# Performance work log

Hardware: AMD Instinct MI355X
Metric: run time of the kernel (lower is better)

The kernel has to match this reference:

```python
import jax, jax.numpy as jnp
import numpy as np

GRAVITY, MAIN_THRUST, SIDE_TORQUE, DT = 10.0, 6.0, 1.0, 0.02
H_OBS = jnp.array([[1, 0, 0, 0, 0, 0],
                   [0, 1, 0, 0, 0, 0],
                   [0, 0, 0, 0, 1, 0]], dtype=jnp.float32)  # (3,6)


def build_psd(log_diag, off_diag, dim):
    rows, cols = np.tril_indices(dim, -1)  # row-major, same order as torch.tril_indices
    L = jnp.zeros((dim, dim), dtype=log_diag.dtype)
    L = L.at[jnp.arange(dim), jnp.arange(dim)].set(jnp.exp(log_diag))
    L = L.at[rows, cols].set(off_diag)
    return L @ L.T + 1e-6 * jnp.eye(dim, dtype=log_diag.dtype)


def setup_inputs() -> dict:
    key = jax.random.key(0)
    B = 524288
    ks = jax.random.split(key, 8)
    z = jax.random.normal(ks[0], (B, 3), dtype=jnp.float32)
    u = jax.random.uniform(ks[1], (B, 2), dtype=jnp.float32)
    x_prev = jax.random.normal(ks[2], (B, 6), dtype=jnp.float32)
    A = 0.1 * jax.random.normal(ks[3], (B, 6, 6), dtype=jnp.float32)
    P_prev = jnp.einsum('bij,bkj->bik', A, A) + 0.5 * jnp.eye(6, dtype=jnp.float32)
    q_log_diag = jnp.array([-3.0, -3.0, -2.0, -2.0, -3.0, -2.0], dtype=jnp.float32)
    q_off_diag = 0.01 * jax.random.normal(ks[4], (15,), dtype=jnp.float32)
    r_log_diag = jnp.array([-2.0, -2.0, -2.0], dtype=jnp.float32)
    r_off_diag = 0.01 * jax.random.normal(ks[5], (3,), dtype=jnp.float32)
    return {"z": z, "u": u, "x_prev": x_prev, "P_prev": P_prev,
            "q_log_diag": q_log_diag, "q_off_diag": q_off_diag,
            "r_log_diag": r_log_diag, "r_off_diag": r_off_diag}


def _dynamics(x, u):
    px, py, vx, vy, theta, omega = (x[:, i] for i in range(6))
    main_power = jnp.clip(u[:, 0], 0.0, 1.0)
    lateral = u[:, 1]
    sin_th, cos_th = jnp.sin(theta), jnp.cos(theta)
    ax = -MAIN_THRUST * sin_th * main_power
    ay = MAIN_THRUST * cos_th * main_power - GRAVITY
    alpha = SIDE_TORQUE * lateral
    new_vx = vx + ax * DT
    new_vy = vy + ay * DT
    new_omega = omega + alpha * DT
    new_px = px + new_vx * DT
    new_py = py + new_vy * DT
    new_theta = theta + new_omega * DT
    return jnp.stack([new_px, new_py, new_vx, new_vy, new_theta, new_omega], axis=-1)


def _dynamics_jacobian(x, u):
    B = x.shape[0]
    theta = x[:, 4]
    main_power = jnp.clip(u[:, 0], 0.0, 1.0)
    sin_th, cos_th = jnp.sin(theta), jnp.cos(theta)
    Tm = MAIN_THRUST * main_power
    d = jnp.arange(6)
    F = jnp.zeros((B, 6, 6), dtype=x.dtype).at[:, d, d].set(1.0)
    F = F.at[:, 0, 2].set(DT).at[:, 1, 3].set(DT).at[:, 4, 5].set(DT)
    F = F.at[:, 2, 4].set(-Tm * cos_th * DT)
    F = F.at[:, 3, 4].set(-Tm * sin_th * DT)
    F = F.at[:, 0, 4].set(-Tm * cos_th * (DT * DT))
    F = F.at[:, 1, 4].set(-Tm * sin_th * (DT * DT))
    return F


def reference(z, u, x_prev, P_prev, q_log_diag, q_off_diag, r_log_diag, r_off_diag):
    Q = build_psd(q_log_diag, q_off_diag, 6)
    R = build_psd(r_log_diag, r_off_diag, 3)
    H = H_OBS
    # predict
    x_pred = _dynamics(x_prev, u)                              # (B,6)
    F = _dynamics_jacobian(x_prev, u)                          # (B,6,6)
    P_pred = jnp.einsum('bij,bjk,blk->bil', F, P_prev, F) + Q  # F P F^T + Q
    # update
    z_pred = jnp.einsum('ij,bj->bi', H, x_pred)                # (B,3)
    y = z - z_pred
    HP = jnp.einsum('ij,bjk->bik', H, P_pred)                  # (B,3,6)
    S = jnp.einsum('bij,kj->bik', HP, H) + R                   # (B,3,3)
    K = jnp.swapaxes(jnp.linalg.solve(S, HP), -1, -2)          # (B,6,3)
    x_upd = x_pred + jnp.einsum('bij,bj->bi', K, y)
    IKH = jnp.eye(6, dtype=x_pred.dtype) - jnp.einsum('bij,jk->bik', K, H)
    P_upd = (jnp.einsum('bij,bjk,blk->bil', IKH, P_pred, IKH)
             + jnp.einsum('bij,jk,blk->bil', K, R, K))          # Joseph form
    return (x_upd, P_upd)
```

## Files before the change

### kernel.cpp

```cpp
#include <hip/hip_runtime.h>

namespace {
constexpr float GRAVITY     = 10.0f;
constexpr float MAIN_THRUST = 6.0f;
constexpr float DT          = 0.02f;
constexpr int   BLK         = 256;
constexpr int   ROWPAD      = 37;
}

__global__ __launch_bounds__(BLK) void ekf_kernel(
    const float* __restrict__ z,
    const float* __restrict__ u,
    const float* __restrict__ x_prev,
    const float* __restrict__ P_prev,
    const float* __restrict__ q_log_diag,
    const float* __restrict__ q_off_diag,
    const float* __restrict__ r_log_diag,
    const float* __restrict__ r_off_diag,
    float* __restrict__ x_out,
    float* __restrict__ P_out,
    int B)
{
    __shared__ float smem[BLK * ROWPAD];

    const int t = threadIdx.x;
    const long long blockElem0 = (long long)blockIdx.x * BLK;
    const long long elemsLeft  = (long long)B - blockElem0;
    const int nElem  = elemsLeft >= BLK ? BLK : (int)elemsLeft;
    const int count4 = nElem * 9;

    {
        const float4* gP4 = reinterpret_cast<const float4*>(P_prev + blockElem0 * 36);
        #pragma unroll
        for (int k = 0; k < 9; ++k) {
            const int g4 = t + k * BLK;
            if (g4 < count4) {
                const float4 v = gP4[g4];
                const int elem = g4 / 9;
                const int off4 = g4 % 9;
                float* dst = &smem[elem * ROWPAD + off4 * 4];
                dst[0] = v.x; dst[1] = v.y; dst[2] = v.z; dst[3] = v.w;
            }
        }
    }
    __syncthreads();

    const bool valid = (t < nElem);
    const long long b = blockElem0 + t;

    if (valid) {
        float L[6][6];
        #pragma unroll
        for (int i = 0; i < 6; ++i)
            #pragma unroll
            for (int j = 0; j < 6; ++j) L[i][j] = 0.0f;
        #pragma unroll
        for (int i = 0; i < 6; ++i) L[i][i] = expf(q_log_diag[i]);
        L[1][0] = q_off_diag[0];
        L[2][0] = q_off_diag[1];  L[2][1] = q_off_diag[2];
        L[3][0] = q_off_diag[3];  L[3][1] = q_off_diag[4];  L[3][2] = q_off_diag[5];
        L[4][0] = q_off_diag[6];  L[4][1] = q_off_diag[7];  L[4][2] = q_off_diag[8];
        L[4][3] = q_off_diag[9];
        L[5][0] = q_off_diag[10]; L[5][1] = q_off_diag[11]; L[5][2] = q_off_diag[12];
        L[5][3] = q_off_diag[13]; L[5][4] = q_off_diag[14];

        float Q[6][6];
        #pragma unroll
        for (int i = 0; i < 6; ++i) {
            #pragma unroll
            for (int j = 0; j <= i; ++j) {
                float s = 0.0f;
                #pragma unroll
                for (int k = 0; k <= j; ++k) s += L[i][k] * L[j][k];
                if (i == j) s += 1e-6f;
                Q[i][j] = s;
                Q[j][i] = s;
            }
        }

        const float rd0 = expf(r_log_diag[0]);
        const float rd1 = expf(r_log_diag[1]);
        const float rd2 = expf(r_log_diag[2]);
        const float ro0 = r_off_diag[0], ro1 = r_off_diag[1], ro2 = r_off_diag[2];
        const float R00 = rd0 * rd0 + 1e-6f;
        const float R10 = ro0 * rd0;
        const float R11 = ro0 * ro0 + rd1 * rd1 + 1e-6f;
        const float R20 = ro1 * rd0;
        const float R21 = ro1 * ro0 + ro2 * rd1;
        const float R22 = ro1 * ro1 + ro2 * ro2 + rd2 * rd2 + 1e-6f;
        const float Rm[3][3] = {{R00, R10, R20}, {R10, R11, R21}, {R20, R21, R22}};

        const float2* xp2 = reinterpret_cast<const float2*>(x_prev + 6 * b);
        const float2 x01 = xp2[0], x23 = xp2[1], x45 = xp2[2];
        const float px = x01.x, py = x01.y, vx = x23.x, vy = x23.y;
        const float th = x45.x, om = x45.y;

        const float2 uu = *reinterpret_cast<const float2*>(u + 2 * b);
        const float mp  = fminf(fmaxf(uu.x, 0.0f), 1.0f);
        const float lat = uu.y;

        float s_th, c_th;
        __sincosf(th, &s_th, &c_th);

        const float Tm  = MAIN_THRUST * mp;
        const float ax  = -Tm * s_th;
        const float ay  =  Tm * c_th - GRAVITY;
        const float nvx = vx + ax * DT;
        const float nvy = vy + ay * DT;
        const float nom = om + lat * DT;
        const float npx = px + nvx * DT;
        const float npy = py + nvy * DT;
        const float nth = th + nom * DT;
        const float xp[6] = {npx, npy, nvx, nvy, nth, nom};

        const float f24 = -Tm * c_th * DT;
        const float f34 = -Tm * s_th * DT;
        const float f04 = f24 * DT;
        const float f14 = f34 * DT;

        float P[36];
        const float* myrow = &smem[t * ROWPAD];
        #pragma unroll
        for (int j = 0; j < 36; ++j) P[j] = myrow[j];

        #pragma unroll
        for (int j = 0; j < 6; ++j) {
            P[0 * 6 + j] += DT * P[2 * 6 + j] + f04 * P[4 * 6 + j];
            P[1 * 6 + j] += DT * P[3 * 6 + j] + f14 * P[4 * 6 + j];
            P[2 * 6 + j] += f24 * P[4 * 6 + j];
            P[3 * 6 + j] += f34 * P[4 * 6 + j];
            P[4 * 6 + j] += DT * P[5 * 6 + j];
        }
        #pragma unroll
        for (int i = 0; i < 6; ++i) {
            const float m0 = P[i * 6 + 0], m1 = P[i * 6 + 1], m2 = P[i * 6 + 2];
            const float m3 = P[i * 6 + 3], m4 = P[i * 6 + 4], m5 = P[i * 6 + 5];
            P[i * 6 + 0] = m0 + DT * m2 + f04 * m4 + Q[i][0];
            P[i * 6 + 1] = m1 + DT * m3 + f14 * m4 + Q[i][1];
            P[i * 6 + 2] = m2 + f24 * m4 + Q[i][2];
            P[i * 6 + 3] = m3 + f34 * m4 + Q[i][3];
            P[i * 6 + 4] = m4 + DT * m5 + Q[i][4];
            P[i * 6 + 5] = m5 + Q[i][5];
        }

        const float* zp = z + 3 * b;
        const float y0 = zp[0] - npx;
        const float y1 = zp[1] - npy;
        const float y2 = zp[2] - nth;

        const float s00 = P[0 * 6 + 0] + Rm[0][0];
        const float s01 = P[0 * 6 + 1] + Rm[0][1];
        const float s02 = P[0 * 6 + 4] + Rm[0][2];
        const float s10 = P[1 * 6 + 0] + Rm[1][0];
        const float s11 = P[1 * 6 + 1] + Rm[1][1];
        const float s12 = P[1 * 6 + 4] + Rm[1][2];
        const float s20 = P[4 * 6 + 0] + Rm[2][0];
        const float s21 = P[4 * 6 + 1] + Rm[2][1];
        const float s22 = P[4 * 6 + 4] + Rm[2][2];

        const float det = s00 * (s11 * s22 - s12 * s21)
                        + s01 * (s12 * s20 - s10 * s22)
                        + s02 * (s10 * s21 - s11 * s20);
        const float invd = 1.0f / det;
        const float i00 = (s11 * s22 - s12 * s21) * invd;
        const float i01 = (s02 * s21 - s01 * s22) * invd;
        const float i02 = (s01 * s12 - s02 * s11) * invd;
        const float i10 = (s12 * s20 - s10 * s22) * invd;
        const float i11 = (s00 * s22 - s02 * s20) * invd;
        const float i12 = (s02 * s10 - s00 * s12) * invd;
        const float i20 = (s10 * s21 - s11 * s20) * invd;
        const float i21 = (s01 * s20 - s00 * s21) * invd;
        const float i22 = (s00 * s11 - s01 * s10) * invd;

        float K[6][3];
        #pragma unroll
        for (int i = 0; i < 6; ++i) {
            const float hp0 = P[0 * 6 + i];
            const float hp1 = P[1 * 6 + i];
            const float hp2 = P[4 * 6 + i];
            K[i][0] = i00 * hp0 + i01 * hp1 + i02 * hp2;
            K[i][1] = i10 * hp0 + i11 * hp1 + i12 * hp2;
            K[i][2] = i20 * hp0 + i21 * hp1 + i22 * hp2;
        }

        float2* xo2 = reinterpret_cast<float2*>(x_out + 6 * b);
        float xu[6];
        #pragma unroll
        for (int i = 0; i < 6; ++i)
            xu[i] = xp[i] + K[i][0] * y0 + K[i][1] * y1 + K[i][2] * y2;
        xo2[0] = make_float2(xu[0], xu[1]);
        xo2[1] = make_float2(xu[2], xu[3]);
        xo2[2] = make_float2(xu[4], xu[5]);

        float r0[6], r1[6], r4[6];
        #pragma unroll
        for (int j = 0; j < 6; ++j) {
            r0[j] = P[0 * 6 + j];
            r1[j] = P[1 * 6 + j];
            r4[j] = P[4 * 6 + j];
        }
        #pragma unroll
        for (int i = 0; i < 6; ++i)
            #pragma unroll
            for (int j = 0; j < 6; ++j)
                P[i * 6 + j] -= K[i][0] * r0[j] + K[i][1] * r1[j] + K[i][2] * r4[j];

        float c0[6], c1[6], c4[6];
        #pragma unroll
        for (int i = 0; i < 6; ++i) {
            c0[i] = P[i * 6 + 0];
            c1[i] = P[i * 6 + 1];
            c4[i] = P[i * 6 + 4];
        }
        float KR[6][3];
        #pragma unroll
        for (int i = 0; i < 6; ++i) {
            #pragma unroll
            for (int a = 0; a < 3; ++a)
                KR[i][a] = K[i][0] * Rm[0][a] + K[i][1] * Rm[1][a] + K[i][2] * Rm[2][a];
        }
        #pragma unroll
        for (int i = 0; i < 6; ++i) {
            #pragma unroll
            for (int j = 0; j < 6; ++j) {
                P[i * 6 + j] += -(c0[i] * K[j][0] + c1[i] * K[j][1] + c4[i] * K[j][2])
                                + (KR[i][0] * K[j][0] + KR[i][1] * K[j][1] + KR[i][2] * K[j][2]);
            }
        }

        float* myrowW = &smem[t * ROWPAD];
        #pragma unroll
        for (int j = 0; j < 36; ++j) myrowW[j] = P[j];
    }
    __syncthreads();

    {
        float4* oP4 = reinterpret_cast<float4*>(P_out + blockElem0 * 36);
        #pragma unroll
        for (int k = 0; k < 9; ++k) {
            const int g4 = t + k * BLK;
            if (g4 < count4) {
                const int elem = g4 / 9;
                const int off4 = g4 % 9;
                const float* src = &smem[elem * ROWPAD + off4 * 4];
                float4 v;
                v.x = src[0]; v.y = src[1]; v.z = src[2]; v.w = src[3];
                oP4[g4] = v;
            }
        }
    }
}

extern "C" void kernel_launch(void* const* d_in, const int* in_sizes, int n_in,
                              void* d_out, int out_size, void* d_ws, size_t ws_size,
                              hipStream_t stream) {
    const float* z          = (const float*)d_in[0];
    const float* u          = (const float*)d_in[1];
    const float* x_prev     = (const float*)d_in[2];
    const float* P_prev     = (const float*)d_in[3];
    const float* q_log_diag = (const float*)d_in[4];
    const float* q_off_diag = (const float*)d_in[5];
    const float* r_log_diag = (const float*)d_in[6];
    const float* r_off_diag = (const float*)d_in[7];

    const int B = in_sizes[0] / 3;
    float* x_out = (float*)d_out;
    float* P_out = (float*)d_out + (size_t)B * 6;

    const int grid = (B + BLK - 1) / BLK;
    ekf_kernel<<<grid, BLK, 0, stream>>>(z, u, x_prev, P_prev,
                                         q_log_diag, q_off_diag,
                                         r_log_diag, r_off_diag,
                                         x_out, P_out, B);
}
```

Measured before the change: 191.7 us.

## Simplify covariance update, precompute Q/R in a separate kernel, vectorize LDS

Replaces the Joseph-form covariance update with the simple (I-KH)P form. The two are algebraically equal for the optimal Kalman gain, so the second 6x6 correction pass is dropped. The per-thread construction of Q and R, including expf calls, moves into a one-thread pre-kernel that writes them to workspace; the main kernel then reads them as uniform loads. Shared-memory rows are padded to 44 floats so they can be read and written as float4, and the block size drops to 128. The trade-offs are an extra kernel launch and slightly different numerical behaviour, since the Joseph form's symmetry and positive-definiteness safeguards are gone.

```diff
diff --git a/kernel.cpp b/kernel.cpp
--- a/kernel.cpp
+++ b/kernel.cpp
@@ -4,8 +4,43 @@
 constexpr float GRAVITY     = 10.0f;
 constexpr float MAIN_THRUST = 6.0f;
 constexpr float DT          = 0.02f;
-constexpr int   BLK         = 256;
-constexpr int   ROWPAD      = 37;
+constexpr int   BLK         = 128;
+constexpr int   ROWPAD      = 44;
+}
+
+__global__ void qr_precompute(const float* __restrict__ qld,
+                              const float* __restrict__ qod,
+                              const float* __restrict__ rld,
+                              const float* __restrict__ rod,
+                              float* __restrict__ out)
+{
+    if (threadIdx.x != 0 || blockIdx.x != 0) return;
+    float L[6][6];
+    for (int i = 0; i < 6; ++i)
+        for (int j = 0; j < 6; ++j) L[i][j] = 0.0f;
+    for (int i = 0; i < 6; ++i) L[i][i] = expf(qld[i]);
+    L[1][0] = qod[0];
+    L[2][0] = qod[1];  L[2][1] = qod[2];
+    L[3][0] = qod[3];  L[3][1] = qod[4];  L[3][2] = qod[5];
+    L[4][0] = qod[6];  L[4][1] = qod[7];  L[4][2] = qod[8];  L[4][3] = qod[9];
+    L[5][0] = qod[10]; L[5][1] = qod[11]; L[5][2] = qod[12]; L[5][3] = qod[13];
+    L[5][4] = qod[14];
+    for (int i = 0; i < 6; ++i)
+        for (int j = 0; j < 6; ++j) {
+            float s = 0.0f;
+            const int m = i < j ? i : j;
+            for (int k = 0; k <= m; ++k) s += L[i][k] * L[j][k];
+            if (i == j) s += 1e-6f;
+            out[i * 6 + j] = s;
+        }
+    const float rd0 = expf(rld[0]), rd1 = expf(rld[1]), rd2 = expf(rld[2]);
+    const float ro0 = rod[0], ro1 = rod[1], ro2 = rod[2];
+    out[36] = rd0 * rd0 + 1e-6f;
+    out[37] = ro0 * rd0;
+    out[38] = ro0 * ro0 + rd1 * rd1 + 1e-6f;
+    out[39] = ro1 * rd0;
+    out[40] = ro1 * ro0 + ro2 * rd1;
+    out[41] = ro1 * ro1 + ro2 * ro2 + rd2 * rd2 + 1e-6f;
 }
 
 __global__ __launch_bounds__(BLK) void ekf_kernel(
@@ -13,10 +48,7 @@
     const float* __restrict__ u,
     const float* __restrict__ x_prev,
     const float* __restrict__ P_prev,
-    const float* __restrict__ q_log_diag,
-    const float* __restrict__ q_off_diag,
-    const float* __restrict__ r_log_diag,
-    const float* __restrict__ r_off_diag,
+    const float* __restrict__ qr,
     float* __restrict__ x_out,
     float* __restrict__ P_out,
     int B)
@@ -38,8 +70,7 @@
                 const float4 v = gP4[g4];
                 const int elem = g4 / 9;
                 const int off4 = g4 % 9;
-                float* dst = &smem[elem * ROWPAD + off4 * 4];
-                dst[0] = v.x; dst[1] = v.y; dst[2] = v.z; dst[3] = v.w;
+                *reinterpret_cast<float4*>(&smem[elem * ROWPAD + off4 * 4]) = v;
             }
         }
     }
@@ -49,46 +80,8 @@
     const long long b = blockElem0 + t;
 
     if (valid) {
-        float L[6][6];
-        #pragma unroll
-        for (int i = 0; i < 6; ++i)
-            #pragma unroll
-            for (int j = 0; j < 6; ++j) L[i][j] = 0.0f;
-        #pragma unroll
-        for (int i = 0; i < 6; ++i) L[i][i] = expf(q_log_diag[i]);
-        L[1][0] = q_off_diag[0];
-        L[2][0] = q_off_diag[1];  L[2][1] = q_off_diag[2];
-        L[3][0] = q_off_diag[3];  L[3][1] = q_off_diag[4];  L[3][2] = q_off_diag[5];
-        L[4][0] = q_off_diag[6];  L[4][1] = q_off_diag[7];  L[4][2] = q_off_diag[8];
-        L[4][3] = q_off_diag[9];
-        L[5][0] = q_off_diag[10]; L[5][1] = q_off_diag[11]; L[5][2] = q_off_diag[12];
-        L[5][3] = q_off_diag[13]; L[5][4] = q_off_diag[14];
-
-        float Q[6][6];
-        #pragma unroll
-        for (int i = 0; i < 6; ++i) {
-            #pragma unroll
-            for (int j = 0; j <= i; ++j) {
-                float s = 0.0f;
-                #pragma unroll
-                for (int k = 0; k <= j; ++k) s += L[i][k] * L[j][k];
-                if (i == j) s += 1e-6f;
-                Q[i][j] = s;
-                Q[j][i] = s;
-            }
-        }
-
-        const float rd0 = expf(r_log_diag[0]);
-        const float rd1 = expf(r_log_diag[1]);
-        const float rd2 = expf(r_log_diag[2]);
-        const float ro0 = r_off_diag[0], ro1 = r_off_diag[1], ro2 = r_off_diag[2];
-        const float R00 = rd0 * rd0 + 1e-6f;
-        const float R10 = ro0 * rd0;
-        const float R11 = ro0 * ro0 + rd1 * rd1 + 1e-6f;
-        const float R20 = ro1 * rd0;
-        const float R21 = ro1 * ro0 + ro2 * rd1;
-        const float R22 = ro1 * ro1 + ro2 * ro2 + rd2 * rd2 + 1e-6f;
-        const float Rm[3][3] = {{R00, R10, R20}, {R10, R11, R21}, {R20, R21, R22}};
+        const float R00 = qr[36], R10 = qr[37], R11 = qr[38];
+        const float R20 = qr[39], R21 = qr[40], R22 = qr[41];
 
         const float2* xp2 = reinterpret_cast<const float2*>(x_prev + 6 * b);
         const float2 x01 = xp2[0], x23 = xp2[1], x45 = xp2[2];
@@ -121,7 +114,11 @@
         float P[36];
         const float* myrow = &smem[t * ROWPAD];
         #pragma unroll
-        for (int j = 0; j < 36; ++j) P[j] = myrow[j];
+        for (int k = 0; k < 9; ++k) {
+            const float4 v = *reinterpret_cast<const float4*>(&myrow[k * 4]);
+            P[4 * k + 0] = v.x; P[4 * k + 1] = v.y;
+            P[4 * k + 2] = v.z; P[4 * k + 3] = v.w;
+        }
 
         #pragma unroll
         for (int j = 0; j < 6; ++j) {
@@ -135,12 +132,12 @@
         for (int i = 0; i < 6; ++i) {
             const float m0 = P[i * 6 + 0], m1 = P[i * 6 + 1], m2 = P[i * 6 + 2];
             const float m3 = P[i * 6 + 3], m4 = P[i * 6 + 4], m5 = P[i * 6 + 5];
-            P[i * 6 + 0] = m0 + DT * m2 + f04 * m4 + Q[i][0];
-            P[i * 6 + 1] = m1 + DT * m3 + f14 * m4 + Q[i][1];
-            P[i * 6 + 2] = m2 + f24 * m4 + Q[i][2];
-            P[i * 6 + 3] = m3 + f34 * m4 + Q[i][3];
-            P[i * 6 + 4] = m4 + DT * m5 + Q[i][4];
-            P[i * 6 + 5] = m5 + Q[i][5];
+            P[i * 6 + 0] = m0 + DT * m2 + f04 * m4 + qr[i * 6 + 0];
+            P[i * 6 + 1] = m1 + DT * m3 + f14 * m4 + qr[i * 6 + 1];
+            P[i * 6 + 2] = m2 + f24 * m4 + qr[i * 6 + 2];
+            P[i * 6 + 3] = m3 + f34 * m4 + qr[i * 6 + 3];
+            P[i * 6 + 4] = m4 + DT * m5 + qr[i * 6 + 4];
+            P[i * 6 + 5] = m5 + qr[i * 6 + 5];
         }
 
         const float* zp = z + 3 * b;
@@ -148,15 +145,15 @@
         const float y1 = zp[1] - npy;
         const float y2 = zp[2] - nth;
 
-        const float s00 = P[0 * 6 + 0] + Rm[0][0];
-        const float s01 = P[0 * 6 + 1] + Rm[0][1];
-        const float s02 = P[0 * 6 + 4] + Rm[0][2];
-        const float s10 = P[1 * 6 + 0] + Rm[1][0];
-        const float s11 = P[1 * 6 + 1] + Rm[1][1];
-        const float s12 = P[1 * 6 + 4] + Rm[1][2];
-        const float s20 = P[4 * 6 + 0] + Rm[2][0];
-        const float s21 = P[4 * 6 + 1] + Rm[2][1];
-        const float s22 = P[4 * 6 + 4] + Rm[2][2];
+        const float s00 = P[0 * 6 + 0] + R00;
+        const float s01 = P[0 * 6 + 1] + R10;
+        const float s02 = P[0 * 6 + 4] + R20;
+        const float s10 = P[1 * 6 + 0] + R10;
+        const float s11 = P[1 * 6 + 1] + R11;
+        const float s12 = P[1 * 6 + 4] + R21;
+        const float s20 = P[4 * 6 + 0] + R20;
+        const float s21 = P[4 * 6 + 1] + R21;
+        const float s22 = P[4 * 6 + 4] + R22;
 
         const float det = s00 * (s11 * s22 - s12 * s21)
                         + s01 * (s12 * s20 - s10 * s22)
@@ -172,12 +169,18 @@
         const float i21 = (s01 * s20 - s00 * s21) * invd;
         const float i22 = (s00 * s11 - s01 * s10) * invd;
 
+        float r0[6], r1[6], r4[6];
+        #pragma unroll
+        for (int j = 0; j < 6; ++j) {
+            r0[j] = P[0 * 6 + j];
+            r1[j] = P[1 * 6 + j];
+            r4[j] = P[4 * 6 + j];
+        }
+
         float K[6][3];
         #pragma unroll
         for (int i = 0; i < 6; ++i) {
-            const float hp0 = P[0 * 6 + i];
-            const float hp1 = P[1 * 6 + i];
-            const float hp2 = P[4 * 6 + i];
+            const float hp0 = r0[i], hp1 = r1[i], hp2 = r4[i];
             K[i][0] = i00 * hp0 + i01 * hp1 + i02 * hp2;
             K[i][1] = i10 * hp0 + i11 * hp1 + i12 * hp2;
             K[i][2] = i20 * hp0 + i21 * hp1 + i22 * hp2;
@@ -192,45 +195,20 @@
         xo2[1] = make_float2(xu[2], xu[3]);
         xo2[2] = make_float2(xu[4], xu[5]);
 
-        float r0[6], r1[6], r4[6];
-        #pragma unroll
-        for (int j = 0; j < 6; ++j) {
-            r0[j] = P[0 * 6 + j];
-            r1[j] = P[1 * 6 + j];
-            r4[j] = P[4 * 6 + j];
-        }
         #pragma unroll
         for (int i = 0; i < 6; ++i)
             #pragma unroll
             for (int j = 0; j < 6; ++j)
                 P[i * 6 + j] -= K[i][0] * r0[j] + K[i][1] * r1[j] + K[i][2] * r4[j];
 
-        float c0[6], c1[6], c4[6];
-        #pragma unroll
-        for (int i = 0; i < 6; ++i) {
-            c0[i] = P[i * 6 + 0];
-            c1[i] = P[i * 6 + 1];
-            c4[i] = P[i * 6 + 4];
-        }
-        float KR[6][3];
-        #pragma unroll
-        for (int i = 0; i < 6; ++i) {
-            #pragma unroll
-            for (int a = 0; a < 3; ++a)
-                KR[i][a] = K[i][0] * Rm[0][a] + K[i][1] * Rm[1][a] + K[i][2] * Rm[2][a];
-        }
-        #pragma unroll
-        for (int i = 0; i < 6; ++i) {
-            #pragma unroll
-            for (int j = 0; j < 6; ++j) {
-                P[i * 6 + j] += -(c0[i] * K[j][0] + c1[i] * K[j][1] + c4[i] * K[j][2])
-                                + (KR[i][0] * K[j][0] + KR[i][1] * K[j][1] + KR[i][2] * K[j][2]);
-            }
-        }
-
         float* myrowW = &smem[t * ROWPAD];
         #pragma unroll
-        for (int j = 0; j < 36; ++j) myrowW[j] = P[j];
+        for (int k = 0; k < 9; ++k) {
+            float4 v;
+            v.x = P[4 * k + 0]; v.y = P[4 * k + 1];
+            v.z = P[4 * k + 2]; v.w = P[4 * k + 3];
+            *reinterpret_cast<float4*>(&myrowW[k * 4]) = v;
+        }
     }
     __syncthreads();
 
@@ -242,10 +220,7 @@
             if (g4 < count4) {
                 const int elem = g4 / 9;
                 const int off4 = g4 % 9;
-                const float* src = &smem[elem * ROWPAD + off4 * 4];
-                float4 v;
-                v.x = src[0]; v.y = src[1]; v.z = src[2]; v.w = src[3];
-                oP4[g4] = v;
+                oP4[g4] = *reinterpret_cast<const float4*>(&smem[elem * ROWPAD + off4 * 4]);
             }
         }
     }
@@ -266,10 +241,12 @@
     const int B = in_sizes[0] / 3;
     float* x_out = (float*)d_out;
     float* P_out = (float*)d_out + (size_t)B * 6;
+    float* qrbuf = (float*)d_ws;
+
+    qr_precompute<<<1, 64, 0, stream>>>(q_log_diag, q_off_diag,
+                                        r_log_diag, r_off_diag, qrbuf);
 
     const int grid = (B + BLK - 1) / BLK;
-    ekf_kernel<<<grid, BLK, 0, stream>>>(z, u, x_prev, P_prev,
-                                         q_log_diag, q_off_diag,
-                                         r_log_diag, r_off_diag,
+    ekf_kernel<<<grid, BLK, 0, stream>>>(z, u, x_prev, P_prev, qrbuf,
                                          x_out, P_out, B);
 }
```

New measurement: 186.4 us. 1.03x faster.
